# Performance work log

Hardware: AMD Instinct MI355X
Metric: run time of the kernel (lower is better)

Reference implementation:

```python
import jax, jax.numpy as jnp
import numpy as np
from jax import lax

D_MODEL = 1024
D_STATE = 16
D_CONV = 4
EXPAND = 2
D_INNER = EXPAND * D_MODEL
DT_RANK = (D_MODEL + 15) // 16  # ceil(d_model/16) = 64
B, L = 2, 2048
EPS = 1e-5


def setup_inputs() -> dict:
    key = jax.random.key(0)
    ks = jax.random.split(key, 12)
    s = 0.02
    inp = {
        "x": jax.random.normal(ks[0], (B, L, D_MODEL), jnp.float32),
        "ln_g": jnp.ones((D_MODEL,), jnp.float32),
        "ln_b": jnp.zeros((D_MODEL,), jnp.float32),
        "sq_w": jax.random.normal(ks[1], (D_MODEL, D_MODEL), jnp.float32) * s,
        "sq_b": jnp.zeros((D_MODEL,), jnp.float32),
        "srw_w": jax.random.normal(ks[2], (D_MODEL, D_MODEL), jnp.float32) * s,
        "srw_b": jnp.zeros((D_MODEL,), jnp.float32),
        "res_scale": jnp.ones((1,), jnp.float32),
        "in_proj_w": jax.random.normal(ks[3], (D_MODEL, 2 * D_INNER), jnp.float32) * s,
        "conv_w": jax.random.normal(ks[4], (D_INNER, D_CONV), jnp.float32) * 0.1,
        "conv_b": jnp.zeros((D_INNER,), jnp.float32),
        "x_proj_w": jax.random.normal(ks[5], (D_INNER, DT_RANK + 2 * D_STATE), jnp.float32) * s,
        "dt_w": jax.random.normal(ks[6], (DT_RANK, D_INNER), jnp.float32) * s,
        "dt_b": jnp.full((D_INNER,), -4.6, jnp.float32),  # softplus(-4.6)~0.01
        "A_log": jnp.log(jnp.broadcast_to(jnp.arange(1, D_STATE + 1, dtype=jnp.float32), (D_INNER, D_STATE))),
        "D": jnp.ones((D_INNER,), jnp.float32),
        "out_proj_w": jax.random.normal(ks[7], (D_INNER, D_MODEL), jnp.float32) * s,
    }
    return inp


def _layernorm(x, g, b):
    mu = jnp.mean(x, axis=-1, keepdims=True)
    var = jnp.mean(jnp.square(x - mu), axis=-1, keepdims=True)
    return (x - mu) * lax.rsqrt(var + EPS) * g + b


def _causal_dwconv(u, w, b):
    # u: [B,L,Din], w: [Din,d_conv] -> causal depthwise conv
    din, dc = w.shape
    up = jnp.pad(u, ((0, 0), (dc - 1, 0), (0, 0)))
    k = w.T[:, None, :]  # [d_conv, 1, Din]
    out = lax.conv_general_dilated(up, k, (1,), "VALID",
                                   dimension_numbers=("NWC", "WIO", "NWC"),
                                   feature_group_count=din)
    return out + b


def _mamba(h, in_proj_w, conv_w, conv_b, x_proj_w, dt_w, dt_b, A_log, D, out_proj_w):
    xz = h @ in_proj_w                       # [B,L,2*Din]
    u, z = jnp.split(xz, 2, axis=-1)
    u = jax.nn.silu(_causal_dwconv(u, conv_w, conv_b))  # [B,L,Din]
    x_dbl = u @ x_proj_w                     # [B,L,R+2N]
    dt, Bm, Cm = jnp.split(x_dbl, [DT_RANK, DT_RANK + D_STATE], axis=-1)
    delta = jax.nn.softplus(dt @ dt_w + dt_b)            # [B,L,Din]
    A = -jnp.exp(A_log)                                  # [Din,N]
    dA = jnp.exp(jnp.einsum("bld,dn->bldn", delta, A))   # [B,L,Din,N]
    dBu = jnp.einsum("bld,bln,bld->bldn", delta, Bm, u)  # [B,L,Din,N]

    def step(hst, inp):
        dA_t, dBu_t, C_t = inp
        hst = dA_t * hst + dBu_t                         # [B,Din,N]
        y = jnp.einsum("bdn,bn->bd", hst, C_t)
        return hst, y

    h0 = jnp.zeros((u.shape[0], D_INNER, D_STATE), u.dtype)
    _, ys = lax.scan(step, h0, (dA.transpose(1, 0, 2, 3),
                                dBu.transpose(1, 0, 2, 3),
                                Cm.transpose(1, 0, 2)))
    y = ys.transpose(1, 0, 2) + u * D                    # [B,L,Din]
    y = y * jax.nn.silu(z)
    return y @ out_proj_w


def reference(x, ln_g, ln_b, sq_w, sq_b, srw_w, srw_b, res_scale,
              in_proj_w, conv_w, conv_b, x_proj_w, dt_w, dt_b, A_log, D, out_proj_w):
    residual = x
    h = _layernorm(x, ln_g, ln_b)
    h = h + (h @ sq_w + sq_b)                # x + spatial_query(x)
    y = _mamba(h, in_proj_w, conv_w, conv_b, x_proj_w, dt_w, dt_b, A_log, D, out_proj_w)
    y = y * (y @ srw_w + srw_b)              # x * spatial_reweight(x)
    return residual + res_scale * y
```

## Files before the change

### kernel.cpp

```cpp
#include <hip/hip_runtime.h>
#include <math.h>


#define DMODEL 1024
#define DINNER 2048
#define NSTATE 16
#define DTRANK 64
#define BATCH  2
#define SEQ    2048
#define ROWS   (BATCH*SEQ)
#define NC     32
#define TS     (SEQ/NC)
#define LN_EPS 1e-5f

typedef unsigned short u16;
typedef __attribute__((ext_vector_type(8))) short bf16x8;
typedef __attribute__((ext_vector_type(4))) float f32x4;

__device__ __forceinline__ float silu_f(float x) { return x / (1.f + __expf(-x)); }

__device__ __forceinline__ u16 f2bf(float f) {
    union { float f; unsigned u; } v; v.f = f;
    unsigned r = v.u + 0x7fffu + ((v.u >> 16) & 1u);
    return (u16)(r >> 16);
}
__device__ __forceinline__ float bf2f(u16 h) {
    union { unsigned u; float f; } v; v.u = ((unsigned)h) << 16; return v.f;
}

__device__ __forceinline__ void gload_lds16(const u16* g, u16* l) {
    __builtin_amdgcn_global_load_lds(
        (const __attribute__((address_space(1))) unsigned int*)(g),
        (__attribute__((address_space(3))) unsigned int*)(static_cast<void*>(l)),
        16, 0, 0);
}

__device__ __forceinline__ void tr_tile(const float* __restrict__ src,
                                        u16* __restrict__ dst,
                                        int R, int C, int xt, int yt, int tx, int ty)
{
    __shared__ float t[32][33];
    int c0 = xt * 32, r0 = yt * 32;
    #pragma unroll
    for (int i = 0; i < 32; i += 8) {
        float v = 0.f;
        if (c0 + tx < C) v = src[(size_t)(r0 + ty + i) * C + c0 + tx];
        t[ty + i][tx] = v;
    }
    __syncthreads();
    #pragma unroll
    for (int i = 0; i < 32; i += 8)
        dst[(size_t)(c0 + ty + i) * R + r0 + tx] = f2bf(t[tx][ty + i]);
}

__global__ __launch_bounds__(256) void prologue_kernel(
    const float* __restrict__ sq_w,  u16* __restrict__ sqT,
    const float* __restrict__ srw_w, u16* __restrict__ srwT,
    const float* __restrict__ inp,   u16* __restrict__ inpT,
    const float* __restrict__ outp,  u16* __restrict__ outpT,
    const float* __restrict__ xp,    u16* __restrict__ xpT,
    const float* __restrict__ dtw,   u16* __restrict__ dtT,
    const float* __restrict__ x,     const float* __restrict__ ln_g,
    const float* __restrict__ ln_b,
    float* __restrict__ h0, u16* __restrict__ h0bf)
{
    int id = blockIdx.x;
    if (id < 8576) {
        int tx = threadIdx.x & 31, ty = threadIdx.x >> 5;
        if (id < 1024)      { tr_tile(sq_w,  sqT,  1024, 1024, id & 31,  id >> 5, tx, ty); }
        else if (id < 2048) { id -= 1024; tr_tile(srw_w, srwT, 1024, 1024, id & 31,  id >> 5, tx, ty); }
        else if (id < 6144) { id -= 2048; tr_tile(inp,  inpT, 1024, 4096, id & 127, id >> 7, tx, ty); }
        else if (id < 8192) { id -= 6144; tr_tile(outp, outpT,2048, 1024, id & 31,  id >> 5, tx, ty); }
        else if (id < 8448) { id -= 8192; tr_tile(xp,   xpT,  2048,   96, id & 3,   id >> 2, tx, ty); }
        else                { id -= 8448; tr_tile(dtw,  dtT,    64, 2048, id & 63,  id >> 6, tx, ty); }
        return;
    }
    int row = id - 8576;
    const float* xr = x + (size_t)row * DMODEL;
    float4 v = ((const float4*)xr)[threadIdx.x];
    float s  = v.x + v.y + v.z + v.w;
    float ss = v.x*v.x + v.y*v.y + v.z*v.z + v.w*v.w;
    #pragma unroll
    for (int off = 32; off; off >>= 1) { s += __shfl_down(s, off); ss += __shfl_down(ss, off); }
    __shared__ float s_s[4], s_ss[4];
    int lane = threadIdx.x & 63, w = threadIdx.x >> 6;
    if (lane == 0) { s_s[w] = s; s_ss[w] = ss; }
    __syncthreads();
    float ts = 0.f, tss = 0.f;
    #pragma unroll
    for (int i = 0; i < 4; i++) { ts += s_s[i]; tss += s_ss[i]; }
    float mu  = ts / (float)DMODEL;
    float var = tss / (float)DMODEL - mu * mu;
    float rstd = rsqrtf(var + LN_EPS);
    float4 gv = ((const float4*)ln_g)[threadIdx.x];
    float4 bv = ((const float4*)ln_b)[threadIdx.x];
    float4 o;
    o.x = (v.x - mu) * rstd * gv.x + bv.x;
    o.y = (v.y - mu) * rstd * gv.y + bv.y;
    o.z = (v.z - mu) * rstd * gv.z + bv.z;
    o.w = (v.w - mu) * rstd * gv.w + bv.w;
    ((float4*)(h0 + (size_t)row * DMODEL))[threadIdx.x] = o;
    unsigned lo = (unsigned)f2bf(o.x) | ((unsigned)f2bf(o.y) << 16);
    unsigned hi = (unsigned)f2bf(o.z) | ((unsigned)f2bf(o.w) << 16);
    ((uint2*)(h0bf + (size_t)row * DMODEL))[threadIdx.x] = make_uint2(lo, hi);
}

__device__ __forceinline__ void stage128(const u16* __restrict__ A, const u16* __restrict__ Bt,
                                         int m0, int n0, int lda, int ldb, int k0,
                                         u16* As, u16* Bs, int tid)
{
    #pragma unroll
    for (int p = 0; p < 2; p++) {
        int idx = p * 256 + tid;
        int row = idx >> 2, seg = idx & 3;
        int ss = seg ^ ((row >> 1) & 3);
        gload_lds16(A  + (size_t)(m0 + row) * lda + k0 + ss * 8, As + idx * 8);
        gload_lds16(Bt + (size_t)(n0 + row) * ldb + k0 + ss * 8, Bs + idx * 8);
    }
}
__device__ __forceinline__ void stage256(const u16* __restrict__ A, const u16* __restrict__ Bt,
                                         int m0, int n0, int lda, int ldb, int k0,
                                         u16* As, u16* Bs, int tid)
{
    #pragma unroll
    for (int p = 0; p < 2; p++) {
        int idx = p * 512 + tid;
        int row = idx >> 2, seg = idx & 3;
        int ss = seg ^ ((row >> 1) & 3);
        gload_lds16(A  + (size_t)(m0 + row) * lda + k0 + ss * 8, As + idx * 8);
        gload_lds16(Bt + (size_t)(n0 + row) * ldb + k0 + ss * 8, Bs + idx * 8);
    }
}

__device__ __forceinline__ void ph128(int t, int nt,
    const u16* __restrict__ A, const u16* __restrict__ Bt,
    int m0, int n0, int lda, int ldb, int tid, int wr, int wc, int g, int r,
    u16* As, u16* Bs, bf16x8 (&avR)[4], bf16x8 (&avW)[4], f32x4 (&acc)[4][4])
{
    if (t + 1 < nt) {
        asm volatile("s_waitcnt vmcnt(0)" ::: "memory");
        __builtin_amdgcn_s_barrier();
        __builtin_amdgcn_sched_barrier(0);
    }
    bf16x8 bv[4];
    {
        const u16* bc = Bs + (t % 3) * 4096;
        #pragma unroll
        for (int ni = 0; ni < 4; ni++) {
            int brow = wc * 64 + ni * 16 + r;
            bv[ni] = *(const bf16x8*)&bc[brow * 32 + ((g ^ ((brow >> 1) & 3)) << 3)];
        }
    }
    __builtin_amdgcn_sched_barrier(0);
    if (t + 1 < nt) {
        const u16* ac = As + ((t + 1) % 3) * 4096;
        #pragma unroll
        for (int mi = 0; mi < 4; mi++) {
            int arow = wr * 64 + mi * 16 + r;
            avW[mi] = *(const bf16x8*)&ac[arow * 32 + ((g ^ ((arow >> 1) & 3)) << 3)];
        }
    }
    if (t + 2 < nt)
        stage128(A, Bt, m0, n0, lda, ldb, (t + 2) << 5,
                 As + ((t + 2) % 3) * 4096, Bs + ((t + 2) % 3) * 4096, tid);
    if (t + 1 < nt) asm volatile("s_waitcnt lgkmcnt(4)" ::: "memory");
    else            asm volatile("s_waitcnt lgkmcnt(0)" ::: "memory");
    __builtin_amdgcn_sched_barrier(0);
    #pragma unroll
    for (int mi = 0; mi < 4; mi++)
        #pragma unroll
        for (int ni = 0; ni < 4; ni++)
            acc[mi][ni] = __builtin_amdgcn_mfma_f32_16x16x32_bf16(avR[mi], bv[ni], acc[mi][ni], 0, 0, 0);
}

__device__ __forceinline__ void ph256(int t, int nt,
    const u16* __restrict__ A, const u16* __restrict__ Bt,
    int m0, int n0, int lda, int ldb, int tid, int wr, int wc, int g, int r,
    u16* As, u16* Bs, bf16x8 (&avR)[8], bf16x8 (&avW)[8], f32x4 (&acc)[8][4])
{
    if (t + 1 < nt) {
        asm volatile("s_waitcnt vmcnt(0)" ::: "memory");
        __builtin_amdgcn_s_barrier();
        __builtin_amdgcn_sched_barrier(0);
    }
    bf16x8 bv[4];
    {
        const u16* bc = Bs + (t % 3) * 8192;
        #pragma unroll
        for (int ni = 0; ni < 4; ni++) {
            int brow = wc * 64 + ni * 16 + r;
            bv[ni] = *(const bf16x8*)&bc[brow * 32 + ((g ^ ((brow >> 1) & 3)) << 3)];
        }
    }
    __builtin_amdgcn_sched_barrier(0);
    if (t + 1 < nt) {
        const u16* ac = As + ((t + 1) % 3) * 8192;
        #pragma unroll
        for (int mi = 0; mi < 8; mi++) {
            int arow = wr * 128 + mi * 16 + r;
            avW[mi] = *(const bf16x8*)&ac[arow * 32 + ((g ^ ((arow >> 1) & 3)) << 3)];
        }
    }
    if (t + 2 < nt)
        stage256(A, Bt, m0, n0, lda, ldb, (t + 2) << 5,
                 As + ((t + 2) % 3) * 8192, Bs + ((t + 2) % 3) * 8192, tid);
    if (t + 1 < nt) asm volatile("s_waitcnt lgkmcnt(8)" ::: "memory");
    else            asm volatile("s_waitcnt lgkmcnt(0)" ::: "memory");
    __builtin_amdgcn_sched_barrier(0);
    __builtin_amdgcn_s_setprio(1);
    #pragma unroll
    for (int mi = 0; mi < 8; mi++)
        #pragma unroll
        for (int ni = 0; ni < 4; ni++)
            acc[mi][ni] = __builtin_amdgcn_mfma_f32_16x16x32_bf16(avR[mi], bv[ni], acc[mi][ni], 0, 0, 0);
    __builtin_amdgcn_s_setprio(0);
}

template<int ACT, bool HAS_BIAS, bool HAS_RES, bool WRITE_BF16, bool WRITE_F32, bool FUSE_FINAL>
__global__ __launch_bounds__(256) void gemm_bf16(
    const u16* __restrict__ A, const u16* __restrict__ Bt,
    float* __restrict__ C, u16* __restrict__ Cbf,
    const float* __restrict__ bias, const float* __restrict__ res,
    const u16* __restrict__ resbf,
    const float* __restrict__ xres, const float* __restrict__ rsp,
    int K, int lda, int ldb, int ldc, int Nout, int splitK)
{
    if (splitK) {
        int sp = blockIdx.z;
        A  += (size_t)sp * splitK;
        Bt += (size_t)sp * splitK;
        C  += (size_t)sp * ROWS * ldc;
        K = splitK;
    }
    __shared__ __align__(16) u16 As[3 * 4096];
    __shared__ __align__(16) u16 Bs[3 * 4096];
    const int tid = threadIdx.x;
    const int wv = tid >> 6, ln = tid & 63;
    const int m0 = blockIdx.y * 128, n0 = blockIdx.x * 128;
    const int g = ln >> 4, r = ln & 15;
    const int wr = wv >> 1, wc = wv & 1;

    f32x4 acc[4][4];
    #pragma unroll
    for (int i = 0; i < 4; i++)
        #pragma unroll
        for (int j = 0; j < 4; j++) acc[i][j] = (f32x4)0.f;

    const int nt = K >> 5;
    stage128(A, Bt, m0, n0, lda, ldb, 0,  As,        Bs,        tid);
    stage128(A, Bt, m0, n0, lda, ldb, 32, As + 4096, Bs + 4096, tid);
    asm volatile("s_waitcnt vmcnt(4)" ::: "memory");
    __builtin_amdgcn_s_barrier();
    __builtin_amdgcn_sched_barrier(0);

    bf16x8 avA[4], avB[4];
    #pragma unroll
    for (int mi = 0; mi < 4; mi++) {
        int arow = wr * 64 + mi * 16 + r;
        avA[mi] = *(const bf16x8*)&As[arow * 32 + ((g ^ ((arow >> 1) & 3)) << 3)];
    }
    for (int tt = 0; tt < nt; tt += 2) {
        ph128(tt,     nt, A, Bt, m0, n0, lda, ldb, tid, wr, wc, g, r, As, Bs, avA, avB, acc);
        ph128(tt + 1, nt, A, Bt, m0, n0, lda, ldb, tid, wr, wc, g, r, As, Bs, avB, avA, acc);
    }

    float rs = FUSE_FINAL ? rsp[0] : 0.f;
    #pragma unroll
    for (int mi = 0; mi < 4; mi++) {
        int row0 = m0 + wr * 64 + mi * 16 + g * 4;
        #pragma unroll
        for (int ni = 0; ni < 4; ni++) {
            int col = n0 + wc * 64 + ni * 16 + r;
            if (col >= Nout) continue;
            float bb = HAS_BIAS ? bias[col] : 0.f;
            #pragma unroll
            for (int j = 0; j < 4; j++) {
                int row = row0 + j;
                float c = acc[mi][ni][j] + bb;
                if (HAS_RES) c += res[(size_t)row * ldc + col];
                if (ACT == 1) c = logf(1.f + __expf(c));
                if (FUSE_FINAL) {
                    float yv = bf2f(resbf[(size_t)row * ldc + col]);
                    c = xres[(size_t)row * ldc + col] + rs * yv * c;
                }
                if (WRITE_F32 || FUSE_FINAL) C[(size_t)row * ldc + col] = c;
                if (WRITE_BF16) Cbf[(size_t)row * ldc + col] = f2bf(c);
            }
        }
    }
}

template<bool ZSILU>
__global__ __launch_bounds__(512, 2) void gemm256_bf16(
    const u16* __restrict__ A, const u16* __restrict__ Bt, u16* __restrict__ Cbf,
    int K, int lda, int ldb, int ldc)
{
    __shared__ __align__(16) u16 As[3 * 8192];
    __shared__ __align__(16) u16 Bs[3 * 8192];
    const int tid = threadIdx.x;
    const int wv = tid >> 6, ln = tid & 63;
    const int g = ln >> 4, r = ln & 15;
    const int wr = wv >> 2, wc = wv & 3;
    const int m0 = blockIdx.y * 256, n0 = blockIdx.x * 256;

    f32x4 acc[8][4];
    #pragma unroll
    for (int i = 0; i < 8; i++)
        #pragma unroll
        for (int j = 0; j < 4; j++) acc[i][j] = (f32x4)0.f;

    const int nt = K >> 5;
    stage256(A, Bt, m0, n0, lda, ldb, 0,  As,        Bs,        tid);
    stage256(A, Bt, m0, n0, lda, ldb, 32, As + 8192, Bs + 8192, tid);
    asm volatile("s_waitcnt vmcnt(4)" ::: "memory");
    __builtin_amdgcn_s_barrier();
    __builtin_amdgcn_sched_barrier(0);

    bf16x8 avA[8], avB[8];
    #pragma unroll
    for (int mi = 0; mi < 8; mi++) {
        int arow = wr * 128 + mi * 16 + r;
        avA[mi] = *(const bf16x8*)&As[arow * 32 + ((g ^ ((arow >> 1) & 3)) << 3)];
    }
    for (int tt = 0; tt < nt; tt += 2) {
        ph256(tt,     nt, A, Bt, m0, n0, lda, ldb, tid, wr, wc, g, r, As, Bs, avA, avB, acc);
        ph256(tt + 1, nt, A, Bt, m0, n0, lda, ldb, tid, wr, wc, g, r, As, Bs, avB, avA, acc);
    }

    const bool isz = ZSILU && (n0 >= DINNER);
    #pragma unroll
    for (int mi = 0; mi < 8; mi++) {
        int row0 = m0 + wr * 128 + mi * 16 + g * 4;
        #pragma unroll
        for (int ni = 0; ni < 4; ni++) {
            int col = n0 + wc * 64 + ni * 16 + r;
            #pragma unroll
            for (int j = 0; j < 4; j++) {
                float c = acc[mi][ni][j];
                if (isz) c = silu_f(c);
                Cbf[(size_t)(row0 + j) * ldc + col] = f2bf(c);
            }
        }
    }
}

__global__ __launch_bounds__(256) void reduce_xproj(const float* __restrict__ part,
                                                    float* __restrict__ xdbl,
                                                    u16* __restrict__ xdbl_bf)
{
    int i = blockIdx.x * 256 + threadIdx.x;
    const int SL = ROWS * 96;
    float s = 0.f;
    #pragma unroll
    for (int k = 0; k < 8; k++) s += part[i + k * SL];
    xdbl[i] = s;
    xdbl_bf[i] = f2bf(s);
}

__global__ __launch_bounds__(256) void conv_silu_kernel(
    const u16* __restrict__ xzbf, const float* __restrict__ w,
    const float* __restrict__ b, u16* __restrict__ u)
{
    int idx = blockIdx.x * 256 + threadIdx.x;
    int d8 = (idx & (DINNER / 8 - 1)) * 8;
    int r  = idx >> 8;
    int t  = r & (SEQ - 1);
    bf16x8 rows[4];
    #pragma unroll
    for (int j = 0; j < 4; j++) {
        int tt = t - 3 + j;
        if (tt >= 0) rows[j] = *(const bf16x8*)&xzbf[(size_t)(r - 3 + j) * 4096 + d8];
        else         rows[j] = (bf16x8)0;
    }
    u16 outv[8];
    #pragma unroll
    for (int e = 0; e < 8; e++) {
        int d = d8 + e;
        float4 wv = *(const float4*)(w + (size_t)d * 4);
        float acc = b[d];
        acc = fmaf(bf2f((u16)rows[0][e]), wv.x, acc);
        acc = fmaf(bf2f((u16)rows[1][e]), wv.y, acc);
        acc = fmaf(bf2f((u16)rows[2][e]), wv.z, acc);
        acc = fmaf(bf2f((u16)rows[3][e]), wv.w, acc);
        outv[e] = f2bf(silu_f(acc));
    }
    *(bf16x8*)&u[(size_t)r * DINNER + d8] = *(const bf16x8*)outv;
}

__global__ __launch_bounds__(256) void scan_phaseA(
    const u16* __restrict__ delta,
    const u16* __restrict__ u,
    const float* __restrict__ xdbl,
    const float* __restrict__ A_log,
    float* __restrict__ S, float* __restrict__ sumdlt)
{
    int d = blockIdx.x * 256 + threadIdx.x;
    int c = blockIdx.y, b = blockIdx.z;
    float Ad[NSTATE];
    #pragma unroll
    for (int n = 0; n < NSTATE; n++) Ad[n] = -__expf(A_log[(size_t)d * NSTATE + n]);
    float hs[NSTATE];
    #pragma unroll
    for (int n = 0; n < NSTATE; n++) hs[n] = 0.f;
    float sd = 0.f;
    int r0 = b * SEQ + c * TS;
    for (int t = 0; t < TS; t++) {
        int r = r0 + t;
        float dlt = bf2f(delta[(size_t)r * DINNER + d]);
        float uu  = bf2f(u[(size_t)r * DINNER + d]);
        const float* bm = xdbl + (size_t)r * 96 + DTRANK;
        float du = dlt * uu;
        sd += dlt;
        #pragma unroll
        for (int n = 0; n < NSTATE; n++) {
            float dA = __expf(dlt * Ad[n]);
            hs[n] = fmaf(dA, hs[n], du * bm[n]);
        }
    }
    size_t base = ((size_t)(b * NC + c) * DINNER + d) * NSTATE;
    #pragma unroll
    for (int n = 0; n < NSTATE; n += 4)
        *(float4*)(S + base + n) = make_float4(hs[n], hs[n+1], hs[n+2], hs[n+3]);
    sumdlt[(size_t)(b * NC + c) * DINNER + d] = sd;
}

__global__ __launch_bounds__(256) void scan_phaseB(
    const float* __restrict__ S, const float* __restrict__ sumdlt,
    const float* __restrict__ A_log, float* __restrict__ Hin)
{
    int idx = blockIdx.x * 256 + threadIdx.x;
    int b  = idx >> 15;
    int dn = idx & (DINNER * NSTATE - 1);
    float Ad = -__expf(A_log[dn]);
    int d = dn >> 4;
    const size_t stride = (size_t)DINNER * NSTATE;
    size_t base  = (size_t)b * NC * stride + dn;
    size_t sbase = (size_t)b * NC * DINNER + d;
    float h = 0.f;
    for (int c = 0; c < NC; c++) {
        size_t off = base + (size_t)c * stride;
        float p = __expf(Ad * sumdlt[sbase + (size_t)c * DINNER]);
        float s = S[off];
        Hin[off] = h;
        h = fmaf(p, h, s);
    }
}

__global__ __launch_bounds__(256) void scan_phaseC(
    const u16* __restrict__ delta,
    u16* __restrict__ u,
    const float* __restrict__ xdbl,
    const float* __restrict__ A_log,
    const float* __restrict__ Hin,
    const float* __restrict__ Dp,
    const u16* __restrict__ xzbf)
{
    int d = blockIdx.x * 256 + threadIdx.x;
    int c = blockIdx.y, b = blockIdx.z;
    float Ad[NSTATE];
    #pragma unroll
    for (int n = 0; n < NSTATE; n++) Ad[n] = -__expf(A_log[(size_t)d * NSTATE + n]);
    float hs[NSTATE];
    size_t hbase = ((size_t)(b * NC + c) * DINNER + d) * NSTATE;
    #pragma unroll
    for (int n = 0; n < NSTATE; n++) hs[n] = Hin[hbase + n];
    float Dd = Dp[d];
    int r0 = b * SEQ + c * TS;
    for (int t = 0; t < TS; t++) {
        int r = r0 + t;
        float dlt = bf2f(delta[(size_t)r * DINNER + d]);
        float uu  = bf2f(u[(size_t)r * DINNER + d]);
        const float* bm = xdbl + (size_t)r * 96 + DTRANK;
        const float* cm = bm + NSTATE;
        float du = dlt * uu;
        float y = 0.f;
        #pragma unroll
        for (int n = 0; n < NSTATE; n++) {
            float dA = __expf(dlt * Ad[n]);
            hs[n] = fmaf(dA, hs[n], du * bm[n]);
            y = fmaf(hs[n], cm[n], y);
        }
        float sz = bf2f(xzbf[(size_t)r * 4096 + DINNER + d]);
        u[(size_t)r * DINNER + d] = f2bf((y + uu * Dd) * sz);
    }
}

extern "C" void kernel_launch(void* const* d_in, const int* in_sizes, int n_in,
                              void* d_out, int out_size, void* d_ws, size_t ws_size,
                              hipStream_t stream)
{
    const float* x         = (const float*)d_in[0];
    const float* ln_g      = (const float*)d_in[1];
    const float* ln_b      = (const float*)d_in[2];
    const float* sq_w      = (const float*)d_in[3];
    const float* sq_b      = (const float*)d_in[4];
    const float* srw_w     = (const float*)d_in[5];
    const float* srw_b     = (const float*)d_in[6];
    const float* res_scale = (const float*)d_in[7];
    const float* in_proj_w = (const float*)d_in[8];
    const float* conv_w    = (const float*)d_in[9];
    const float* conv_b    = (const float*)d_in[10];
    const float* x_proj_w  = (const float*)d_in[11];
    const float* dt_w      = (const float*)d_in[12];
    const float* dt_b      = (const float*)d_in[13];
    const float* A_log     = (const float*)d_in[14];
    const float* Dp        = (const float*)d_in[15];
    const float* out_proj_w= (const float*)d_in[16];
    float* out = (float*)d_out;

    char* ws = (char*)d_ws;
    float* h0      = (float*)(ws + 0);
    u16*   delta_bf= (u16*)  (ws + 0);
    float* xpart   = (float*)(ws + ((size_t)16 << 20));
    u16*   xz_bf   = (u16*)  (ws + ((size_t)32 << 20));
    u16*   u_bf    = (u16*)  (ws + ((size_t)64 << 20));
    float* xdbl    = (float*)(ws + ((size_t)80 << 20));
    u16*   xprojT  = (u16*)  (ws + ((size_t)82 << 20));
    u16*   h0_bf   = (u16*)  (ws + ((size_t)83 << 20));
    u16*   xdbl_bf = (u16*)  (ws + ((size_t)83 << 20));
    u16*   h_bf    = (u16*)  (ws + ((size_t)91 << 20));
    float* sumdlt  = (float*)(ws + ((size_t)91 << 20));
    float* S       = (float*)(ws + ((size_t)99 << 20));
    u16*   y2_bf   = (u16*)  (ws + ((size_t)99 << 20));
    float* Hin     = (float*)(ws + ((size_t)115 << 20));
    u16*   sqT     = (u16*)  (ws + ((size_t)131 << 20));
    u16*   srwT    = (u16*)  (ws + ((size_t)133 << 20));
    u16*   inprojT = (u16*)  (ws + ((size_t)135 << 20));
    u16*   outprojT= (u16*)  (ws + ((size_t)143 << 20));
    u16*   dtT     = (u16*)  (ws + ((size_t)147 << 20));

    dim3 blk(256);

    prologue_kernel<<<8576 + ROWS, blk, 0, stream>>>(
        sq_w, sqT, srw_w, srwT, in_proj_w, inprojT, out_proj_w, outprojT,
        x_proj_w, xprojT, dt_w, dtT, x, ln_g, ln_b, h0, h0_bf);
    gemm_bf16<0, true, true, true, false, false><<<dim3(8, 32), blk, 0, stream>>>(
        h0_bf, sqT, nullptr, h_bf, sq_b, h0, nullptr, nullptr, nullptr,
        DMODEL, DMODEL, DMODEL, DMODEL, DMODEL, 0);
    gemm256_bf16<true><<<dim3(16, 16), dim3(512), 0, stream>>>(
        h_bf, inprojT, xz_bf, DMODEL, DMODEL, DMODEL, 2 * DINNER);
    conv_silu_kernel<<<(ROWS * DINNER / 8) / 256, blk, 0, stream>>>(xz_bf, conv_w, conv_b, u_bf);
    gemm_bf16<0, false, false, false, true, false><<<dim3(1, 32, 8), blk, 0, stream>>>(
        u_bf, xprojT, xpart, nullptr, nullptr, nullptr, nullptr, nullptr, nullptr,
        DINNER, DINNER, DINNER, 96, 96, DINNER / 8);
    reduce_xproj<<<(ROWS * 96) / 256, blk, 0, stream>>>(xpart, xdbl, xdbl_bf);
    gemm_bf16<1, true, false, true, false, false><<<dim3(16, 32), blk, 0, stream>>>(
        xdbl_bf, dtT, nullptr, delta_bf, dt_b, nullptr, nullptr, nullptr, nullptr,
        DTRANK, 96, DTRANK, DINNER, DINNER, 0);
    scan_phaseA<<<dim3(DINNER / 256, NC, BATCH), blk, 0, stream>>>(delta_bf, u_bf, xdbl, A_log, S, sumdlt);
    scan_phaseB<<<dim3((BATCH * DINNER * NSTATE) / 256), blk, 0, stream>>>(S, sumdlt, A_log, Hin);
    scan_phaseC<<<dim3(DINNER / 256, NC, BATCH), blk, 0, stream>>>(delta_bf, u_bf, xdbl, A_log, Hin, Dp, xz_bf);
    gemm_bf16<0, false, false, true, false, false><<<dim3(8, 32), blk, 0, stream>>>(
        u_bf, outprojT, nullptr, y2_bf, nullptr, nullptr, nullptr, nullptr, nullptr,
        DINNER, DINNER, DINNER, DMODEL, DMODEL, 0);
    gemm_bf16<0, true, false, false, false, true><<<dim3(8, 32), blk, 0, stream>>>(
        y2_bf, srwT, out, nullptr, srw_b, nullptr, y2_bf, x, res_scale,
        DMODEL, DMODEL, DMODEL, DMODEL, DMODEL, 0);
}
```

Baseline: 273.9 us.

## Use 8-wave 128x128 GEMM blocks and drop fp32 LayerNorm output buffer

Measured after the change: 261.2 us. 4.6% less time.

```diff
diff --git a/kernel.cpp b/kernel.cpp
--- a/kernel.cpp
+++ b/kernel.cpp
@@ -62,7 +62,7 @@
     const float* __restrict__ dtw,   u16* __restrict__ dtT,
     const float* __restrict__ x,     const float* __restrict__ ln_g,
     const float* __restrict__ ln_b,
-    float* __restrict__ h0, u16* __restrict__ h0bf)
+    u16* __restrict__ h0bf)
 {
     int id = blockIdx.x;
     if (id < 8576) {
@@ -99,24 +99,19 @@
     o.y = (v.y - mu) * rstd * gv.y + bv.y;
     o.z = (v.z - mu) * rstd * gv.z + bv.z;
     o.w = (v.w - mu) * rstd * gv.w + bv.w;
-    ((float4*)(h0 + (size_t)row * DMODEL))[threadIdx.x] = o;
     unsigned lo = (unsigned)f2bf(o.x) | ((unsigned)f2bf(o.y) << 16);
     unsigned hi = (unsigned)f2bf(o.z) | ((unsigned)f2bf(o.w) << 16);
     ((uint2*)(h0bf + (size_t)row * DMODEL))[threadIdx.x] = make_uint2(lo, hi);
 }
 
-__device__ __forceinline__ void stage128(const u16* __restrict__ A, const u16* __restrict__ Bt,
-                                         int m0, int n0, int lda, int ldb, int k0,
-                                         u16* As, u16* Bs, int tid)
-{
-    #pragma unroll
-    for (int p = 0; p < 2; p++) {
-        int idx = p * 256 + tid;
-        int row = idx >> 2, seg = idx & 3;
-        int ss = seg ^ ((row >> 1) & 3);
-        gload_lds16(A  + (size_t)(m0 + row) * lda + k0 + ss * 8, As + idx * 8);
-        gload_lds16(Bt + (size_t)(n0 + row) * ldb + k0 + ss * 8, Bs + idx * 8);
-    }
+__device__ __forceinline__ void stage128w8(const u16* __restrict__ A, const u16* __restrict__ Bt,
+                                           int m0, int n0, int lda, int ldb, int k0,
+                                           u16* As, u16* Bs, int tid)
+{
+    int row = tid >> 2, seg = tid & 3;
+    int ss = seg ^ ((row >> 1) & 3);
+    gload_lds16(A  + (size_t)(m0 + row) * lda + k0 + ss * 8, As + tid * 8);
+    gload_lds16(Bt + (size_t)(n0 + row) * ldb + k0 + ss * 8, Bs + tid * 8);
 }
 __device__ __forceinline__ void stage256(const u16* __restrict__ A, const u16* __restrict__ Bt,
                                          int m0, int n0, int lda, int ldb, int k0,
@@ -132,22 +127,22 @@
     }
 }
 
-__device__ __forceinline__ void ph128(int t, int nt,
+__device__ __forceinline__ void ph128w8(int t, int nt,
     const u16* __restrict__ A, const u16* __restrict__ Bt,
     int m0, int n0, int lda, int ldb, int tid, int wr, int wc, int g, int r,
-    u16* As, u16* Bs, bf16x8 (&avR)[4], bf16x8 (&avW)[4], f32x4 (&acc)[4][4])
+    u16* As, u16* Bs, bf16x8 (&avR)[4], bf16x8 (&avW)[4], f32x4 (&acc)[4][2])
 {
     if (t + 1 < nt) {
         asm volatile("s_waitcnt vmcnt(0)" ::: "memory");
         __builtin_amdgcn_s_barrier();
         __builtin_amdgcn_sched_barrier(0);
     }
-    bf16x8 bv[4];
+    bf16x8 bv[2];
     {
         const u16* bc = Bs + (t % 3) * 4096;
         #pragma unroll
-        for (int ni = 0; ni < 4; ni++) {
-            int brow = wc * 64 + ni * 16 + r;
+        for (int ni = 0; ni < 2; ni++) {
+            int brow = wc * 32 + ni * 16 + r;
             bv[ni] = *(const bf16x8*)&bc[brow * 32 + ((g ^ ((brow >> 1) & 3)) << 3)];
         }
     }
@@ -161,15 +156,15 @@
         }
     }
     if (t + 2 < nt)
-        stage128(A, Bt, m0, n0, lda, ldb, (t + 2) << 5,
-                 As + ((t + 2) % 3) * 4096, Bs + ((t + 2) % 3) * 4096, tid);
+        stage128w8(A, Bt, m0, n0, lda, ldb, (t + 2) << 5,
+                   As + ((t + 2) % 3) * 4096, Bs + ((t + 2) % 3) * 4096, tid);
     if (t + 1 < nt) asm volatile("s_waitcnt lgkmcnt(4)" ::: "memory");
     else            asm volatile("s_waitcnt lgkmcnt(0)" ::: "memory");
     __builtin_amdgcn_sched_barrier(0);
     #pragma unroll
     for (int mi = 0; mi < 4; mi++)
         #pragma unroll
-        for (int ni = 0; ni < 4; ni++)
+        for (int ni = 0; ni < 2; ni++)
             acc[mi][ni] = __builtin_amdgcn_mfma_f32_16x16x32_bf16(avR[mi], bv[ni], acc[mi][ni], 0, 0, 0);
 }
 
@@ -217,10 +212,10 @@
 }
 
 template<int ACT, bool HAS_BIAS, bool HAS_RES, bool WRITE_BF16, bool WRITE_F32, bool FUSE_FINAL>
-__global__ __launch_bounds__(256) void gemm_bf16(
+__global__ __launch_bounds__(512, 2) void gemm_bf16(
     const u16* __restrict__ A, const u16* __restrict__ Bt,
     float* __restrict__ C, u16* __restrict__ Cbf,
-    const float* __restrict__ bias, const float* __restrict__ res,
+    const float* __restrict__ bias,
     const u16* __restrict__ resbf,
     const float* __restrict__ xres, const float* __restrict__ rsp,
     int K, int lda, int ldb, int ldc, int Nout, int splitK)
@@ -238,18 +233,18 @@
     const int wv = tid >> 6, ln = tid & 63;
     const int m0 = blockIdx.y * 128, n0 = blockIdx.x * 128;
     const int g = ln >> 4, r = ln & 15;
-    const int wr = wv >> 1, wc = wv & 1;
-
-    f32x4 acc[4][4];
+    const int wr = wv >> 2, wc = wv & 3;
+
+    f32x4 acc[4][2];
     #pragma unroll
     for (int i = 0; i < 4; i++)
         #pragma unroll
-        for (int j = 0; j < 4; j++) acc[i][j] = (f32x4)0.f;
+        for (int j = 0; j < 2; j++) acc[i][j] = (f32x4)0.f;
 
     const int nt = K >> 5;
-    stage128(A, Bt, m0, n0, lda, ldb, 0,  As,        Bs,        tid);
-    stage128(A, Bt, m0, n0, lda, ldb, 32, As + 4096, Bs + 4096, tid);
-    asm volatile("s_waitcnt vmcnt(4)" ::: "memory");
+    stage128w8(A, Bt, m0, n0, lda, ldb, 0,  As,        Bs,        tid);
+    stage128w8(A, Bt, m0, n0, lda, ldb, 32, As + 4096, Bs + 4096, tid);
+    asm volatile("s_waitcnt vmcnt(2)" ::: "memory");
     __builtin_amdgcn_s_barrier();
     __builtin_amdgcn_sched_barrier(0);
 
@@ -260,8 +255,8 @@
         avA[mi] = *(const bf16x8*)&As[arow * 32 + ((g ^ ((arow >> 1) & 3)) << 3)];
     }
     for (int tt = 0; tt < nt; tt += 2) {
-        ph128(tt,     nt, A, Bt, m0, n0, lda, ldb, tid, wr, wc, g, r, As, Bs, avA, avB, acc);
-        ph128(tt + 1, nt, A, Bt, m0, n0, lda, ldb, tid, wr, wc, g, r, As, Bs, avB, avA, acc);
+        ph128w8(tt,     nt, A, Bt, m0, n0, lda, ldb, tid, wr, wc, g, r, As, Bs, avA, avB, acc);
+        ph128w8(tt + 1, nt, A, Bt, m0, n0, lda, ldb, tid, wr, wc, g, r, As, Bs, avB, avA, acc);
     }
 
     float rs = FUSE_FINAL ? rsp[0] : 0.f;
@@ -269,15 +264,15 @@
     for (int mi = 0; mi < 4; mi++) {
         int row0 = m0 + wr * 64 + mi * 16 + g * 4;
         #pragma unroll
-        for (int ni = 0; ni < 4; ni++) {
-            int col = n0 + wc * 64 + ni * 16 + r;
+        for (int ni = 0; ni < 2; ni++) {
+            int col = n0 + wc * 32 + ni * 16 + r;
             if (col >= Nout) continue;
             float bb = HAS_BIAS ? bias[col] : 0.f;
             #pragma unroll
             for (int j = 0; j < 4; j++) {
                 int row = row0 + j;
                 float c = acc[mi][ni][j] + bb;
-                if (HAS_RES) c += res[(size_t)row * ldc + col];
+                if (HAS_RES) c += bf2f(resbf[(size_t)row * ldc + col]);
                 if (ACT == 1) c = logf(1.f + __expf(c));
                 if (FUSE_FINAL) {
                     float yv = bf2f(resbf[(size_t)row * ldc + col]);
@@ -509,7 +504,6 @@
     float* out = (float*)d_out;
 
     char* ws = (char*)d_ws;
-    float* h0      = (float*)(ws + 0);
     u16*   delta_bf= (u16*)  (ws + 0);
     float* xpart   = (float*)(ws + ((size_t)16 << 20));
     u16*   xz_bf   = (u16*)  (ws + ((size_t)32 << 20));
@@ -517,43 +511,43 @@
     float* xdbl    = (float*)(ws + ((size_t)80 << 20));
     u16*   xprojT  = (u16*)  (ws + ((size_t)82 << 20));
     u16*   h0_bf   = (u16*)  (ws + ((size_t)83 << 20));
-    u16*   xdbl_bf = (u16*)  (ws + ((size_t)83 << 20));
-    u16*   h_bf    = (u16*)  (ws + ((size_t)91 << 20));
+    u16*   xdbl_bf = (u16*)  (ws + ((size_t)83 << 20) + (8 << 20));
+    u16*   h_bf    = (u16*)  (ws + ((size_t)91 << 20) + (1 << 20));
     float* sumdlt  = (float*)(ws + ((size_t)91 << 20));
-    float* S       = (float*)(ws + ((size_t)99 << 20));
-    u16*   y2_bf   = (u16*)  (ws + ((size_t)99 << 20));
-    float* Hin     = (float*)(ws + ((size_t)115 << 20));
-    u16*   sqT     = (u16*)  (ws + ((size_t)131 << 20));
-    u16*   srwT    = (u16*)  (ws + ((size_t)133 << 20));
-    u16*   inprojT = (u16*)  (ws + ((size_t)135 << 20));
-    u16*   outprojT= (u16*)  (ws + ((size_t)143 << 20));
-    u16*   dtT     = (u16*)  (ws + ((size_t)147 << 20));
-
-    dim3 blk(256);
+    float* S       = (float*)(ws + ((size_t)100 << 20));
+    u16*   y2_bf   = (u16*)  (ws + ((size_t)100 << 20));
+    float* Hin     = (float*)(ws + ((size_t)116 << 20));
+    u16*   sqT     = (u16*)  (ws + ((size_t)132 << 20));
+    u16*   srwT    = (u16*)  (ws + ((size_t)134 << 20));
+    u16*   inprojT = (u16*)  (ws + ((size_t)136 << 20));
+    u16*   outprojT= (u16*)  (ws + ((size_t)144 << 20));
+    u16*   dtT     = (u16*)  (ws + ((size_t)148 << 20));
+
+    dim3 blk(256), blk8(512);
 
     prologue_kernel<<<8576 + ROWS, blk, 0, stream>>>(
         sq_w, sqT, srw_w, srwT, in_proj_w, inprojT, out_proj_w, outprojT,
-        x_proj_w, xprojT, dt_w, dtT, x, ln_g, ln_b, h0, h0_bf);
-    gemm_bf16<0, true, true, true, false, false><<<dim3(8, 32), blk, 0, stream>>>(
-        h0_bf, sqT, nullptr, h_bf, sq_b, h0, nullptr, nullptr, nullptr,
+        x_proj_w, xprojT, dt_w, dtT, x, ln_g, ln_b, h0_bf);
+    gemm_bf16<0, true, true, true, false, false><<<dim3(8, 32), blk8, 0, stream>>>(
+        h0_bf, sqT, nullptr, h_bf, sq_b, h0_bf, nullptr, nullptr,
         DMODEL, DMODEL, DMODEL, DMODEL, DMODEL, 0);
-    gemm256_bf16<true><<<dim3(16, 16), dim3(512), 0, stream>>>(
+    gemm256_bf16<true><<<dim3(16, 16), blk8, 0, stream>>>(
         h_bf, inprojT, xz_bf, DMODEL, DMODEL, DMODEL, 2 * DINNER);
     conv_silu_kernel<<<(ROWS * DINNER / 8) / 256, blk, 0, stream>>>(xz_bf, conv_w, conv_b, u_bf);
-    gemm_bf16<0, false, false, false, true, false><<<dim3(1, 32, 8), blk, 0, stream>>>(
-        u_bf, xprojT, xpart, nullptr, nullptr, nullptr, nullptr, nullptr, nullptr,
+    gemm_bf16<0, false, false, false, true, false><<<dim3(1, 32, 8), blk8, 0, stream>>>(
+        u_bf, xprojT, xpart, nullptr, nullptr, nullptr, nullptr, nullptr,
         DINNER, DINNER, DINNER, 96, 96, DINNER / 8);
     reduce_xproj<<<(ROWS * 96) / 256, blk, 0, stream>>>(xpart, xdbl, xdbl_bf);
-    gemm_bf16<1, true, false, true, false, false><<<dim3(16, 32), blk, 0, stream>>>(
-        xdbl_bf, dtT, nullptr, delta_bf, dt_b, nullptr, nullptr, nullptr, nullptr,
+    gemm_bf16<1, true, false, true, false, false><<<dim3(16, 32), blk8, 0, stream>>>(
+        xdbl_bf, dtT, nullptr, delta_bf, dt_b, nullptr, nullptr, nullptr,
         DTRANK, 96, DTRANK, DINNER, DINNER, 0);
     scan_phaseA<<<dim3(DINNER / 256, NC, BATCH), blk, 0, stream>>>(delta_bf, u_bf, xdbl, A_log, S, sumdlt);
     scan_phaseB<<<dim3((BATCH * DINNER * NSTATE) / 256), blk, 0, stream>>>(S, sumdlt, A_log, Hin);
     scan_phaseC<<<dim3(DINNER / 256, NC, BATCH), blk, 0, stream>>>(delta_bf, u_bf, xdbl, A_log, Hin, Dp, xz_bf);
-    gemm_bf16<0, false, false, true, false, false><<<dim3(8, 32), blk, 0, stream>>>(
-        u_bf, outprojT, nullptr, y2_bf, nullptr, nullptr, nullptr, nullptr, nullptr,
+    gemm_bf16<0, false, false, true, false, false><<<dim3(8, 32), blk8, 0, stream>>>(
+        u_bf, outprojT, nullptr, y2_bf, nullptr, nullptr, nullptr, nullptr,
         DINNER, DINNER, DINNER, DMODEL, DMODEL, 0);
-    gemm_bf16<0, true, false, false, false, true><<<dim3(8, 32), blk, 0, stream>>>(
-        y2_bf, srwT, out, nullptr, srw_b, nullptr, y2_bf, x, res_scale,
+    gemm_bf16<0, true, false, false, false, true><<<dim3(8, 32), blk8, 0, stream>>>(
+        y2_bf, srwT, out, nullptr, srw_b, y2_bf, x, res_scale,
         DMODEL, DMODEL, DMODEL, DMODEL, DMODEL, 0);
 }
```
